# Kernel optimization log

Hardware: AMD Instinct MI355X
Metric: run time of the kernel (lower is better)

## Reference

```python
import jax, jax.numpy as jnp
import numpy as np

B, S, D, H = 4, 2048, 512, 8
DEPTH = D // H


def setup_inputs() -> dict:
    key = jax.random.key(0)
    ks = jax.random.split(key, 12)
    s = 0.02
    return {
        "q": jax.random.normal(ks[0], (B, S, D), jnp.float32),
        "k": jax.random.normal(ks[1], (B, S, D), jnp.float32),
        "v": jax.random.normal(ks[2], (B, S, D), jnp.float32),
        "mask": jax.random.randint(ks[3], (B, 1, 1, S), 0, 2, jnp.int32),
        "wq": jax.random.normal(ks[4], (D, D), jnp.float32) * s,
        "bq": jnp.zeros((D,), jnp.float32),
        "wk": jax.random.normal(ks[5], (D, D), jnp.float32) * s,
        "bk": jnp.zeros((D,), jnp.float32),
        "wv": jax.random.normal(ks[6], (D, D), jnp.float32) * s,
        "bv": jnp.zeros((D,), jnp.float32),
        "wo": jax.random.normal(ks[7], (D, D), jnp.float32) * s,
        "bo": jnp.zeros((D,), jnp.float32),
    }


def _split_heads(x):
    # [B,S,D] -> [B,H,S,depth]
    b = x.shape[0]
    return x.reshape(b, -1, H, DEPTH).transpose(0, 2, 1, 3)


def reference(q, k, v, mask, wq, bq, wk, bk, wv, bv, wo, bo):
    qh = _split_heads(q @ wq + bq)
    kh = _split_heads(k @ wk + bk)
    vh = _split_heads(v @ wv + bv)
    scale = 1.0 / jnp.sqrt(jnp.float32(DEPTH))
    logits = jnp.einsum("bhqd,bhkd->bhqk", qh, kh) * scale
    logits = logits + mask.astype(jnp.float32) * -1e9
    attn = jax.nn.softmax(logits, axis=-1)  # [B,H,Sq,Sk]
    out = jnp.einsum("bhqk,bhkd->bhqd", attn, vh)
    out = out.transpose(0, 2, 1, 3).reshape(q.shape[0], -1, D)
    out = out @ wo + bo
    return out, attn
```

## Files before the change

kernel.cpp:

```cpp
#include <hip/hip_runtime.h>

#define B_ 4
#define S_ 2048
#define D_ 512
#define H_ 8
#define DP_ 64
#define NT_ (S_/64)

typedef __attribute__((ext_vector_type(4))) float f32x4;
typedef __attribute__((ext_vector_type(8))) short short8;
typedef __attribute__((ext_vector_type(4))) int i32x4;

__device__ __forceinline__ short f2bf(float f){
  unsigned u = __float_as_uint(f);
  u += 0x7fff + ((u >> 16) & 1);
  return (short)(u >> 16);
}

__device__ __forceinline__ int cvtpk(float lo, float hi){
  int r;
  asm("v_cvt_pk_bf16_f32 %0, %1, %2" : "=v"(r) : "v"(lo), "v"(hi));
  return r;
}

#define SWZ(r, kb) ((r)*64 + ((kb) ^ (((r)&7)<<3)))
#define F2(r) ((((r)&3)) | ((((r)>>3)&1)<<2))
#define SWZ2(r, kb) ((r)*64 + ((kb) ^ (F2(r)<<3)))

#define WAITV(N) do{ asm volatile("s_waitcnt vmcnt(" #N ")" ::: "memory"); }while(0)
#define BAR() do{ __builtin_amdgcn_s_barrier(); __builtin_amdgcn_sched_barrier(0); }while(0)

template<int NC>
__device__ __forceinline__ void stage_swz(const short* __restrict__ g, int rowStride,
                                          short* shbase, int w, int l){
  #pragma unroll
  for(int i = 0; i < NC; ++i){
    int byte = (w*NC + i)*1024 + l*16;
    int row = byte >> 7;
    int gs = ((byte >> 4) & 7) ^ (row & 7);
    const short* src = g + (size_t)row*rowStride + gs*8;
    __builtin_amdgcn_global_load_lds((const __attribute__((address_space(1))) void*)src,
        (__attribute__((address_space(3))) void*)(shbase + (w*NC + i)*512), 16, 0, 0);
  }
}
template<int NC>
__device__ __forceinline__ void stage_swz2(const short* __restrict__ g, int rowStride,
                                           short* shbase, int w, int l){
  #pragma unroll
  for(int i = 0; i < NC; ++i){
    int byte = (w*NC + i)*1024 + l*16;
    int row = byte >> 7;
    int gs = ((byte >> 4) & 7) ^ F2(row);
    const short* src = g + (size_t)row*rowStride + gs*8;
    __builtin_amdgcn_global_load_lds((const __attribute__((address_space(1))) void*)src,
        (__attribute__((address_space(3))) void*)(shbase + (w*NC + i)*512), 16, 0, 0);
  }
}

__global__ __launch_bounds__(256) void k_pre(const int* __restrict__ mask,
        const float* __restrict__ w0, const float* __restrict__ w1,
        const float* __restrict__ w2, const float* __restrict__ w3,
        short* __restrict__ wT, float* __restrict__ mb){
  __shared__ float tt[32][33];
  const int bi = blockIdx.x, t = threadIdx.x;
  if(bi < 1024){
    const int z = bi >> 8;
    const float* w = z == 0 ? w0 : z == 1 ? w1 : z == 2 ? w2 : w3;
    short* wt = wT + z * 262144;
    const int bxy = bi & 255;
    const int bx = (bxy & 15) * 32, by = (bxy >> 4) * 32;
    const int tx = t & 31, ty = t >> 5;
    #pragma unroll
    for(int i = 0; i < 32; i += 8) tt[ty + i][tx] = w[(by + ty + i) * D_ + bx + tx];
    __syncthreads();
    #pragma unroll
    for(int i = 0; i < 32; i += 8) wt[(bx + ty + i) * D_ + by + tx] = f2bf(tt[tx][ty + i]);
  } else {
    int i = (bi - 1024) * 256 + t;
    mb[i] = mask[i] ? -1.0e9f : 0.0f;
  }
}

__global__ __launch_bounds__(256) void k_gemm_qkv(const float* __restrict__ qf,
        const float* __restrict__ kf, const float* __restrict__ vf,
        const short* __restrict__ WTall, const float* __restrict__ b0,
        const float* __restrict__ b1, const float* __restrict__ b2,
        short* __restrict__ qh, short* __restrict__ kh, short* __restrict__ vvt){
  __shared__ __align__(16) short As[8192];
  __shared__ __align__(16) short Bs[8192];
  const int z = blockIdx.z;
  const float* X = z == 0 ? qf : (z == 1 ? kf : vf);
  const short* WT = WTall + (size_t)z * (D_*D_);
  const float* bias = z==0 ? b0 : (z==1 ? b1 : b2);
  const int t = threadIdx.x, l = t & 63, w = t >> 6;
  const int lr = l & 15, lg = l >> 4;
  const int m0 = blockIdx.x * 128, n0 = blockIdx.y * 128;
  const int wr = w >> 1, wc = w & 1;
  const float* Xb = X + (size_t)m0 * D_;
  const short* Wb = WT + (size_t)n0 * D_;
  f32x4 acc[4][4] = {};
  for(int kt = 0; kt < D_ / 64; ++kt){
    #pragma unroll
    for(int i = 0; i < 4; ++i){
      int e = t + 256 * i;
      int row = e >> 3, c8 = (e & 7) * 8;
      const float* src = Xb + (size_t)row * D_ + kt * 64 + c8;
      float4 f0 = *reinterpret_cast<const float4*>(src);
      float4 f1 = *reinterpret_cast<const float4*>(src + 4);
      i32x4 pk;
      pk[0] = cvtpk(f0.x, f0.y); pk[1] = cvtpk(f0.z, f0.w);
      pk[2] = cvtpk(f1.x, f1.y); pk[3] = cvtpk(f1.z, f1.w);
      *reinterpret_cast<i32x4*>(&As[SWZ(row, c8)]) = pk;
    }
    stage_swz<4>(Wb + kt*64, D_, Bs, w, l);
    __syncthreads();
    #pragma unroll
    for(int ks = 0; ks < 2; ++ks){
      const int kb = ks*32 + lg*8;
      short8 a[4], b[4];
      #pragma unroll
      for(int mt = 0; mt < 4; ++mt)
        a[mt] = *reinterpret_cast<const short8*>(&As[SWZ(wr*64 + mt*16 + lr, kb)]);
      #pragma unroll
      for(int nt = 0; nt < 4; ++nt)
        b[nt] = *reinterpret_cast<const short8*>(&Bs[SWZ(wc*64 + nt*16 + lr, kb)]);
      __builtin_amdgcn_s_setprio(1);
      #pragma unroll
      for(int mt = 0; mt < 4; ++mt)
        #pragma unroll
        for(int nt = 0; nt < 4; ++nt)
          acc[mt][nt] = __builtin_amdgcn_mfma_f32_16x16x32_bf16(a[mt], b[nt], acc[mt][nt], 0, 0, 0);
      __builtin_amdgcn_s_setprio(0);
    }
    __syncthreads();
  }
  #pragma unroll
  for(int mt = 0; mt < 4; ++mt){
    #pragma unroll
    for(int nt = 0; nt < 4; ++nt){
      const int n = n0 + wc*64 + nt*16 + lr;
      const int m4 = m0 + wr*64 + mt*16 + lg*4;
      float vals[4];
      #pragma unroll
      for(int r = 0; r < 4; ++r) vals[r] = acc[mt][nt][r] + bias[n];
      if(z == 2){
        short4 pv4;
        pv4.x = f2bf(vals[0]); pv4.y = f2bf(vals[1]); pv4.z = f2bf(vals[2]); pv4.w = f2bf(vals[3]);
        *reinterpret_cast<short4*>(&vvt[
            (((size_t)((m4 >> 11) * H_ + (n >> 6))) * DP_ + (n & 63)) * S_ + (m4 & 2047)]) = pv4;
      } else {
        short* dst = z == 0 ? qh : kh;
        #pragma unroll
        for(int r = 0; r < 4; ++r){
          int m = m4 + r;
          dst[(((size_t)((m >> 11) * H_ + (n >> 6))) * S_ + (m & 2047)) * DP_ + (n & 63)] = f2bf(vals[r]);
        }
      }
    }
  }
}

__global__ __launch_bounds__(256) void k_gemm_out(const short* __restrict__ X,
        const short* __restrict__ WT, const float* __restrict__ bias,
        float* __restrict__ Out){
  __shared__ __align__(16) short As[8192];
  __shared__ __align__(16) short Bs[8192];
  const int t = threadIdx.x, l = t & 63, w = t >> 6;
  const int lr = l & 15, lg = l >> 4;
  const int m0 = blockIdx.x * 128, n0 = blockIdx.y * 128;
  const int wr = w >> 1, wc = w & 1;
  const short* Xb = X + (size_t)m0 * D_;
  const short* Wb = WT + (size_t)n0 * D_;
  f32x4 acc[4][4] = {};
  for(int kt = 0; kt < D_ / 64; ++kt){
    stage_swz<4>(Xb + kt*64, D_, As, w, l);
    stage_swz<4>(Wb + kt*64, D_, Bs, w, l);
    __syncthreads();
    #pragma unroll
    for(int ks = 0; ks < 2; ++ks){
      const int kb = ks*32 + lg*8;
      short8 a[4], b[4];
      #pragma unroll
      for(int mt = 0; mt < 4; ++mt)
        a[mt] = *reinterpret_cast<const short8*>(&As[SWZ(wr*64 + mt*16 + lr, kb)]);
      #pragma unroll
      for(int nt = 0; nt < 4; ++nt)
        b[nt] = *reinterpret_cast<const short8*>(&Bs[SWZ(wc*64 + nt*16 + lr, kb)]);
      __builtin_amdgcn_s_setprio(1);
      #pragma unroll
      for(int mt = 0; mt < 4; ++mt)
        #pragma unroll
        for(int nt = 0; nt < 4; ++nt)
          acc[mt][nt] = __builtin_amdgcn_mfma_f32_16x16x32_bf16(a[mt], b[nt], acc[mt][nt], 0, 0, 0);
      __builtin_amdgcn_s_setprio(0);
    }
    __syncthreads();
  }
  #pragma unroll
  for(int mt = 0; mt < 4; ++mt){
    #pragma unroll
    for(int nt = 0; nt < 4; ++nt){
      const int n = n0 + wc*64 + nt*16 + lr;
      const int m4 = m0 + wr*64 + mt*16 + lg*4;
      #pragma unroll
      for(int r = 0; r < 4; ++r)
        Out[(size_t)(m4 + r) * D_ + n] = acc[mt][nt][r] + bias[n];
    }
  }
}

__global__ __launch_bounds__(512, 2) void k_attn(const short* __restrict__ qh,
                                                 const short* __restrict__ kh,
                                                 const short* __restrict__ vt,
                                                 const float* __restrict__ mb,
                                                 float* __restrict__ attn,
                                                 short* __restrict__ ctx){
  __shared__ __align__(16) short Sh[45056];
  const int t = threadIdx.x, l = t & 63, w = t >> 6;
  const int lr = l & 15, lg = l >> 4;
  int lin = blockIdx.y * 8 + blockIdx.x;
  int sw = (lin & 7) * 32 + (lin >> 3);
  const int bh = sw >> 3, b = bh >> 3, h = bh & 7;
  const int q0 = (sw & 7) * 256;
  const short* Qb = qh + (size_t)bh * S_ * DP_ + (size_t)q0 * DP_;
  const short* Kb = kh + (size_t)bh * S_ * DP_;
  const short* Vtb = vt + (size_t)bh * DP_ * S_;
  const float* Mbb = mb + b * S_;
  float* Mlds = (float*)Sh;
  short* KA = Sh + 4096;
  short* KB = Sh + 4096;
  short* VB = Sh + 20480;
  short* Qs = Sh + 28672;
  const float scale = 0.125f;

  __builtin_amdgcn_global_load_lds(
      (const __attribute__((address_space(1))) void*)(Mbb + w*256 + l*4),
      (__attribute__((address_space(3))) void*)(Mlds + w*256 + l*4), 16, 0, 0);
  stage_swz2<4>(Qb, DP_, Qs, w, l);
  stage_swz2<1>(Kb,          DP_, KA,          w, l);
  stage_swz2<1>(Kb + 4096,   DP_, KA + 4096,   w, l);
  stage_swz2<1>(Kb + 2*4096, DP_, KA + 2*4096, w, l);
  stage_swz2<1>(Kb + 3*4096, DP_, KA + 3*4096, w, l);
  WAITV(4); BAR();
  short8 bq[2][2];
  #pragma unroll
  for(int qs = 0; qs < 2; ++qs){
    int r = w * 32 + qs * 16 + lr;
    bq[qs][0] = *reinterpret_cast<const short8*>(&Qs[SWZ2(r, lg * 8)]);
    bq[qs][1] = *reinterpret_cast<const short8*>(&Qs[SWZ2(r, 32 + lg * 8)]);
  }
  const int grow = ((lr >> 2) << 3) + (lr & 3);

  float ps[2] = {0.f, 0.f};
  for(int i = 0; i < NT_/2; ++i){
    if(i < NT_/2 - 1){ WAITV(2); } else { WAITV(0); }
    BAR();
    if(i + 2 < NT_/2){
      int tfa = 2*i + 4, tfb = 2*i + 5;
      stage_swz2<1>(Kb + (size_t)tfa * 4096, DP_, KA + (tfa % 6) * 4096, w, l);
      stage_swz2<1>(Kb + (size_t)tfb * 4096, DP_, KA + (tfb % 6) * 4096, w, l);
    }
    #pragma unroll
    for(int tt = 0; tt < 2; ++tt){
      const int kt = 2*i + tt;
      const short* Kc = KA + (kt % 6) * 4096;
      const float* Ml = Mlds + kt * 64;
      #pragma unroll
      for(int st = 0; st < 4; ++st){
        const int ks = st >> 1, h4 = st & 1;
        const int row = grow + h4 * 4 + ks * 32;
        const int mcol = ks * 32 + h4 * 4 + lg * 8;
        const float4 mv = *(const float4*)&Ml[mcol];
        short8 ak0 = *reinterpret_cast<const short8*>(&Kc[SWZ2(row, lg * 8)]);
        short8 ak1 = *reinterpret_cast<const short8*>(&Kc[SWZ2(row, 32 + lg * 8)]);
        __builtin_amdgcn_s_setprio(1);
        f32x4 c0 = {}, c1 = {};
        c0 = __builtin_amdgcn_mfma_f32_16x16x32_bf16(ak0, bq[0][0], c0, 0, 0, 0);
        c0 = __builtin_amdgcn_mfma_f32_16x16x32_bf16(ak1, bq[0][1], c0, 0, 0, 0);
        c1 = __builtin_amdgcn_mfma_f32_16x16x32_bf16(ak0, bq[1][0], c1, 0, 0, 0);
        c1 = __builtin_amdgcn_mfma_f32_16x16x32_bf16(ak1, bq[1][1], c1, 0, 0, 0);
        __builtin_amdgcn_s_setprio(0);
        ps[0] += __expf(__builtin_fmaf(c0[0], scale, mv.x));
        ps[0] += __expf(__builtin_fmaf(c0[1], scale, mv.y));
        ps[0] += __expf(__builtin_fmaf(c0[2], scale, mv.z));
        ps[0] += __expf(__builtin_fmaf(c0[3], scale, mv.w));
        ps[1] += __expf(__builtin_fmaf(c1[0], scale, mv.x));
        ps[1] += __expf(__builtin_fmaf(c1[1], scale, mv.y));
        ps[1] += __expf(__builtin_fmaf(c1[2], scale, mv.z));
        ps[1] += __expf(__builtin_fmaf(c1[3], scale, mv.w));
      }
    }
  }
  #pragma unroll
  for(int qs = 0; qs < 2; ++qs){
    ps[qs] += __shfl_xor(ps[qs], 16, 64);
    ps[qs] += __shfl_xor(ps[qs], 32, 64);
  }
  const float rinv0 = 1.f / ps[0], rinv1 = 1.f / ps[1];

  BAR();
  stage_swz2<1>(Kb,          DP_, KB,          w, l);
  stage_swz2<1>(Kb + 4096,   DP_, KB + 4096,   w, l);
  stage_swz2<1>(Vtb,         S_,  VB,          w, l);
  stage_swz2<1>(Vtb + 64,    S_,  VB + 4096,   w, l);
  stage_swz2<1>(Kb + 2*4096, DP_, KB + 2*4096, w, l);
  stage_swz2<1>(Kb + 3*4096, DP_, KB + 3*4096, w, l);
  stage_swz2<1>(Vtb + 2*64,  S_,  VB + 2*4096, w, l);
  stage_swz2<1>(Vtb + 3*64,  S_,  VB + 3*4096, w, l);

  f32x4 o[2][4] = {};
  for(int i = 0; i < NT_/2; ++i){
    if(i == 0){ WAITV(4); } else { WAITV(16); }
    BAR();
    if(i >= 1 && i + 1 < NT_/2){
      int tfa = 2*i + 2, tfb = 2*i + 3;
      stage_swz2<1>(Kb + (size_t)tfa * 4096, DP_, KB + (tfa & 3) * 4096, w, l);
      stage_swz2<1>(Kb + (size_t)tfb * 4096, DP_, KB + (tfb & 3) * 4096, w, l);
      stage_swz2<1>(Vtb + (size_t)tfa * 64,  S_,  VB + (tfa & 3) * 4096, w, l);
      stage_swz2<1>(Vtb + (size_t)tfb * 64,  S_,  VB + (tfb & 3) * 4096, w, l);
    }
    #pragma unroll
    for(int tt = 0; tt < 2; ++tt){
      const int kt = 2*i + tt;
      const short* Kc = KB + (kt & 3) * 4096;
      const short* Vc = VB + (kt & 3) * 4096;
      const float* Ml = Mlds + kt * 64;
      i32x4 pav[2][2];
      #pragma unroll
      for(int st = 0; st < 4; ++st){
        const int ks = st >> 1, h4 = st & 1;
        const int row = grow + h4 * 4 + ks * 32;
        const int mcol = ks * 32 + h4 * 4 + lg * 8;
        const float4 mv = *(const float4*)&Ml[mcol];
        short8 ak0 = *reinterpret_cast<const short8*>(&Kc[SWZ2(row, lg * 8)]);
        short8 ak1 = *reinterpret_cast<const short8*>(&Kc[SWZ2(row, 32 + lg * 8)]);
        __builtin_amdgcn_s_setprio(1);
        f32x4 c0 = {}, c1 = {};
        c0 = __builtin_amdgcn_mfma_f32_16x16x32_bf16(ak0, bq[0][0], c0, 0, 0, 0);
        c0 = __builtin_amdgcn_mfma_f32_16x16x32_bf16(ak1, bq[0][1], c0, 0, 0, 0);
        c1 = __builtin_amdgcn_mfma_f32_16x16x32_bf16(ak0, bq[1][0], c1, 0, 0, 0);
        c1 = __builtin_amdgcn_mfma_f32_16x16x32_bf16(ak1, bq[1][1], c1, 0, 0, 0);
        __builtin_amdgcn_s_setprio(0);
        float4 pw0, pw1;
        pw0.x = __expf(__builtin_fmaf(c0[0], scale, mv.x)) * rinv0;
        pw0.y = __expf(__builtin_fmaf(c0[1], scale, mv.y)) * rinv0;
        pw0.z = __expf(__builtin_fmaf(c0[2], scale, mv.z)) * rinv0;
        pw0.w = __expf(__builtin_fmaf(c0[3], scale, mv.w)) * rinv0;
        pw1.x = __expf(__builtin_fmaf(c1[0], scale, mv.x)) * rinv1;
        pw1.y = __expf(__builtin_fmaf(c1[1], scale, mv.y)) * rinv1;
        pw1.z = __expf(__builtin_fmaf(c1[2], scale, mv.z)) * rinv1;
        pw1.w = __expf(__builtin_fmaf(c1[3], scale, mv.w)) * rinv1;
        const int q0r = q0 + w * 32 + lr;
        *reinterpret_cast<float4*>(&attn[((size_t)bh * S_ + q0r) * S_ + kt * 64 + mcol]) = pw0;
        *reinterpret_cast<float4*>(&attn[((size_t)bh * S_ + q0r + 16) * S_ + kt * 64 + mcol]) = pw1;
        pav[0][ks][h4 * 2 + 0] = cvtpk(pw0.x, pw0.y);
        pav[0][ks][h4 * 2 + 1] = cvtpk(pw0.z, pw0.w);
        pav[1][ks][h4 * 2 + 0] = cvtpk(pw1.x, pw1.y);
        pav[1][ks][h4 * 2 + 1] = cvtpk(pw1.z, pw1.w);
      }
      #pragma unroll
      for(int ks = 0; ks < 2; ++ks){
        short8 pa0 = __builtin_bit_cast(short8, pav[0][ks]);
        short8 pa1 = __builtin_bit_cast(short8, pav[1][ks]);
        __builtin_amdgcn_s_setprio(1);
        #pragma unroll
        for(int dt = 0; dt < 4; ++dt){
          short8 vb = *reinterpret_cast<const short8*>(&Vc[SWZ2(dt * 16 + lr, ks * 32 + lg * 8)]);
          o[0][dt] = __builtin_amdgcn_mfma_f32_16x16x32_bf16(pa0, vb, o[0][dt], 0, 0, 0);
          o[1][dt] = __builtin_amdgcn_mfma_f32_16x16x32_bf16(pa1, vb, o[1][dt], 0, 0, 0);
        }
        __builtin_amdgcn_s_setprio(0);
      }
    }
  }
  #pragma unroll
  for(int qs = 0; qs < 2; ++qs){
    #pragma unroll
    for(int dt = 0; dt < 4; ++dt){
      #pragma unroll
      for(int r = 0; r < 4; ++r){
        int q = q0 + w * 32 + qs * 16 + lg * 4 + r;
        int dd = h * 64 + dt * 16 + lr;
        ctx[((size_t)b * S_ + q) * D_ + dd] = f2bf(o[qs][dt][r]);
      }
    }
  }
}

extern "C" void kernel_launch(void* const* d_in, const int* in_sizes, int n_in,
                              void* d_out, int out_size, void* d_ws, size_t ws_size,
                              hipStream_t stream){
  const float* q  = (const float*)d_in[0];
  const float* k  = (const float*)d_in[1];
  const float* v  = (const float*)d_in[2];
  const int* mask = (const int*)d_in[3];
  const float* wq = (const float*)d_in[4];
  const float* bq = (const float*)d_in[5];
  const float* wk = (const float*)d_in[6];
  const float* bk = (const float*)d_in[7];
  const float* wv = (const float*)d_in[8];
  const float* bv = (const float*)d_in[9];
  const float* wo = (const float*)d_in[10];
  const float* bo = (const float*)d_in[11];

  float* out  = (float*)d_out;
  float* attn = out + (size_t)B_ * S_ * D_;

  char* ws = (char*)d_ws;
  short* qh  = (short*)(ws);
  short* kh  = (short*)(ws + 8388608);
  short* vvt = (short*)(ws + 16777216);
  short* ctx = (short*)(ws + 25165824);
  short* wT  = (short*)(ws + 33554432);
  float* mb  = (float*)(ws + 33554432 + 4 * 524288);

  hipLaunchKernelGGL(k_pre, dim3(1056), dim3(256), 0, stream,
                     mask, wq, wk, wv, wo, wT, mb);

  hipLaunchKernelGGL(k_gemm_qkv, dim3(64, 4, 3), dim3(256), 0, stream,
                     q, k, v, wT, bq, bk, bv, qh, kh, vvt);

  hipLaunchKernelGGL(k_attn, dim3(8, 32), dim3(512), 0, stream, qh, kh, vvt, mb, attn, ctx);

  hipLaunchKernelGGL(k_gemm_out, dim3(64, 4), dim3(256), 0, stream, ctx, wT + 3 * 262144, bo, out);
}
```

Before: 251.5 us.

## Split key tiles across two warp groups and halve query tile per block

The attention kernel now processes 128 queries per block instead of 256. Its 8 warps form two groups that take alternating key tiles, so twice as many blocks launch. Row-sum partials and the output accumulators are combined across the two groups through LDS. The launch bound rises to 4 blocks per CU and LDS use drops. The aim is better occupancy and more parallelism across CUs, at the cost of extra LDS reductions, barriers and redundant K/V staging per block.

Result: faster. 223.0 us (-11.3%).

```diff
diff --git a/kernel.cpp b/kernel.cpp
--- a/kernel.cpp
+++ b/kernel.cpp
@@ -28,6 +28,7 @@
 #define SWZ2(r, kb) ((r)*64 + ((kb) ^ (F2(r)<<3)))
 
 #define WAITV(N) do{ asm volatile("s_waitcnt vmcnt(" #N ")" ::: "memory"); }while(0)
+#define WAITLGKM() do{ asm volatile("s_waitcnt lgkmcnt(0)" ::: "memory"); }while(0)
 #define BAR() do{ __builtin_amdgcn_s_barrier(); __builtin_amdgcn_sched_barrier(0); }while(0)
 
 template<int NC>
@@ -209,19 +210,20 @@
   }
 }
 
-__global__ __launch_bounds__(512, 2) void k_attn(const short* __restrict__ qh,
+__global__ __launch_bounds__(512, 4) void k_attn(const short* __restrict__ qh,
                                                  const short* __restrict__ kh,
                                                  const short* __restrict__ vt,
                                                  const float* __restrict__ mb,
                                                  float* __restrict__ attn,
                                                  short* __restrict__ ctx){
-  __shared__ __align__(16) short Sh[45056];
+  __shared__ __align__(16) short Sh[37376];
   const int t = threadIdx.x, l = t & 63, w = t >> 6;
   const int lr = l & 15, lg = l >> 4;
-  int lin = blockIdx.y * 8 + blockIdx.x;
-  int sw = (lin & 7) * 32 + (lin >> 3);
-  const int bh = sw >> 3, b = bh >> 3, h = bh & 7;
-  const int q0 = (sw & 7) * 256;
+  const int wq = w & 3, g = w >> 2;
+  int lin = blockIdx.y * 16 + blockIdx.x;
+  int sw = (lin & 7) * 64 + (lin >> 3);
+  const int bh = sw >> 4, b = bh >> 3, h = bh & 7;
+  const int q0 = (sw & 15) * 128;
   const short* Qb = qh + (size_t)bh * S_ * DP_ + (size_t)q0 * DP_;
   const short* Kb = kh + (size_t)bh * S_ * DP_;
   const short* Vtb = vt + (size_t)bh * DP_ * S_;
@@ -231,12 +233,13 @@
   short* KB = Sh + 4096;
   short* VB = Sh + 20480;
   short* Qs = Sh + 28672;
+  float* Ps_ = (float*)(Sh + 36864);
   const float scale = 0.125f;
 
   __builtin_amdgcn_global_load_lds(
       (const __attribute__((address_space(1))) void*)(Mbb + w*256 + l*4),
       (__attribute__((address_space(3))) void*)(Mlds + w*256 + l*4), 16, 0, 0);
-  stage_swz2<4>(Qb, DP_, Qs, w, l);
+  stage_swz2<2>(Qb, DP_, Qs, w, l);
   stage_swz2<1>(Kb,          DP_, KA,          w, l);
   stage_swz2<1>(Kb + 4096,   DP_, KA + 4096,   w, l);
   stage_swz2<1>(Kb + 2*4096, DP_, KA + 2*4096, w, l);
@@ -245,13 +248,13 @@
   short8 bq[2][2];
   #pragma unroll
   for(int qs = 0; qs < 2; ++qs){
-    int r = w * 32 + qs * 16 + lr;
+    int r = wq * 32 + qs * 16 + lr;
     bq[qs][0] = *reinterpret_cast<const short8*>(&Qs[SWZ2(r, lg * 8)]);
     bq[qs][1] = *reinterpret_cast<const short8*>(&Qs[SWZ2(r, 32 + lg * 8)]);
   }
   const int grow = ((lr >> 2) << 3) + (lr & 3);
 
-  float ps[2] = {0.f, 0.f};
+  float ps2[2] = {0.f, 0.f};
   for(int i = 0; i < NT_/2; ++i){
     if(i < NT_/2 - 1){ WAITV(2); } else { WAITV(0); }
     BAR();
@@ -260,45 +263,42 @@
       stage_swz2<1>(Kb + (size_t)tfa * 4096, DP_, KA + (tfa % 6) * 4096, w, l);
       stage_swz2<1>(Kb + (size_t)tfb * 4096, DP_, KA + (tfb % 6) * 4096, w, l);
     }
-    #pragma unroll
-    for(int tt = 0; tt < 2; ++tt){
-      const int kt = 2*i + tt;
-      const short* Kc = KA + (kt % 6) * 4096;
-      const float* Ml = Mlds + kt * 64;
-      #pragma unroll
-      for(int st = 0; st < 4; ++st){
-        const int ks = st >> 1, h4 = st & 1;
-        const int row = grow + h4 * 4 + ks * 32;
-        const int mcol = ks * 32 + h4 * 4 + lg * 8;
-        const float4 mv = *(const float4*)&Ml[mcol];
-        short8 ak0 = *reinterpret_cast<const short8*>(&Kc[SWZ2(row, lg * 8)]);
-        short8 ak1 = *reinterpret_cast<const short8*>(&Kc[SWZ2(row, 32 + lg * 8)]);
-        __builtin_amdgcn_s_setprio(1);
-        f32x4 c0 = {}, c1 = {};
-        c0 = __builtin_amdgcn_mfma_f32_16x16x32_bf16(ak0, bq[0][0], c0, 0, 0, 0);
-        c0 = __builtin_amdgcn_mfma_f32_16x16x32_bf16(ak1, bq[0][1], c0, 0, 0, 0);
-        c1 = __builtin_amdgcn_mfma_f32_16x16x32_bf16(ak0, bq[1][0], c1, 0, 0, 0);
-        c1 = __builtin_amdgcn_mfma_f32_16x16x32_bf16(ak1, bq[1][1], c1, 0, 0, 0);
-        __builtin_amdgcn_s_setprio(0);
-        ps[0] += __expf(__builtin_fmaf(c0[0], scale, mv.x));
-        ps[0] += __expf(__builtin_fmaf(c0[1], scale, mv.y));
-        ps[0] += __expf(__builtin_fmaf(c0[2], scale, mv.z));
-        ps[0] += __expf(__builtin_fmaf(c0[3], scale, mv.w));
-        ps[1] += __expf(__builtin_fmaf(c1[0], scale, mv.x));
-        ps[1] += __expf(__builtin_fmaf(c1[1], scale, mv.y));
-        ps[1] += __expf(__builtin_fmaf(c1[2], scale, mv.z));
-        ps[1] += __expf(__builtin_fmaf(c1[3], scale, mv.w));
-      }
+    const int kt = 2*i + g;
+    const short* Kc = KA + (kt % 6) * 4096;
+    const float* Ml = Mlds + kt * 64;
+    #pragma unroll
+    for(int st = 0; st < 4; ++st){
+      const int ks = st >> 1, h4 = st & 1;
+      const int row = grow + h4 * 4 + ks * 32;
+      const int mcol = ks * 32 + h4 * 4 + lg * 8;
+      const float4 mv = *(const float4*)&Ml[mcol];
+      short8 ak0 = *reinterpret_cast<const short8*>(&Kc[SWZ2(row, lg * 8)]);
+      short8 ak1 = *reinterpret_cast<const short8*>(&Kc[SWZ2(row, 32 + lg * 8)]);
+      __builtin_amdgcn_s_setprio(1);
+      f32x4 c0 = {}, c1 = {};
+      c0 = __builtin_amdgcn_mfma_f32_16x16x32_bf16(ak0, bq[0][0], c0, 0, 0, 0);
+      c0 = __builtin_amdgcn_mfma_f32_16x16x32_bf16(ak1, bq[0][1], c0, 0, 0, 0);
+      c1 = __builtin_amdgcn_mfma_f32_16x16x32_bf16(ak0, bq[1][0], c1, 0, 0, 0);
+      c1 = __builtin_amdgcn_mfma_f32_16x16x32_bf16(ak1, bq[1][1], c1, 0, 0, 0);
+      __builtin_amdgcn_s_setprio(0);
+      ps2[0] += __expf(__builtin_fmaf(c0[0], scale, mv.x));
+      ps2[0] += __expf(__builtin_fmaf(c0[1], scale, mv.y));
+      ps2[0] += __expf(__builtin_fmaf(c0[2], scale, mv.z));
+      ps2[0] += __expf(__builtin_fmaf(c0[3], scale, mv.w));
+      ps2[1] += __expf(__builtin_fmaf(c1[0], scale, mv.x));
+      ps2[1] += __expf(__builtin_fmaf(c1[1], scale, mv.y));
+      ps2[1] += __expf(__builtin_fmaf(c1[2], scale, mv.z));
+      ps2[1] += __expf(__builtin_fmaf(c1[3], scale, mv.w));
     }
   }
   #pragma unroll
   for(int qs = 0; qs < 2; ++qs){
-    ps[qs] += __shfl_xor(ps[qs], 16, 64);
-    ps[qs] += __shfl_xor(ps[qs], 32, 64);
-  }
-  const float rinv0 = 1.f / ps[0], rinv1 = 1.f / ps[1];
-
-  BAR();
+    ps2[qs] += __shfl_xor(ps2[qs], 16, 64);
+    ps2[qs] += __shfl_xor(ps2[qs], 32, 64);
+  }
+  Ps_[(w*2 + 0)*16 + lr] = ps2[0];
+  Ps_[(w*2 + 1)*16 + lr] = ps2[1];
+  WAITLGKM(); BAR();
   stage_swz2<1>(Kb,          DP_, KB,          w, l);
   stage_swz2<1>(Kb + 4096,   DP_, KB + 4096,   w, l);
   stage_swz2<1>(Vtb,         S_,  VB,          w, l);
@@ -307,10 +307,12 @@
   stage_swz2<1>(Kb + 3*4096, DP_, KB + 3*4096, w, l);
   stage_swz2<1>(Vtb + 2*64,  S_,  VB + 2*4096, w, l);
   stage_swz2<1>(Vtb + 3*64,  S_,  VB + 3*4096, w, l);
+  const float rinv0 = 1.f / (ps2[0] + Ps_[((w^4)*2 + 0)*16 + lr]);
+  const float rinv1 = 1.f / (ps2[1] + Ps_[((w^4)*2 + 1)*16 + lr]);
 
   f32x4 o[2][4] = {};
   for(int i = 0; i < NT_/2; ++i){
-    if(i == 0){ WAITV(4); } else { WAITV(16); }
+    if(i == 0){ WAITV(4); } else { WAITV(8); }
     BAR();
     if(i >= 1 && i + 1 < NT_/2){
       int tfa = 2*i + 2, tfb = 2*i + 3;
@@ -319,69 +321,82 @@
       stage_swz2<1>(Vtb + (size_t)tfa * 64,  S_,  VB + (tfa & 3) * 4096, w, l);
       stage_swz2<1>(Vtb + (size_t)tfb * 64,  S_,  VB + (tfb & 3) * 4096, w, l);
     }
-    #pragma unroll
-    for(int tt = 0; tt < 2; ++tt){
-      const int kt = 2*i + tt;
-      const short* Kc = KB + (kt & 3) * 4096;
-      const short* Vc = VB + (kt & 3) * 4096;
-      const float* Ml = Mlds + kt * 64;
-      i32x4 pav[2][2];
-      #pragma unroll
-      for(int st = 0; st < 4; ++st){
-        const int ks = st >> 1, h4 = st & 1;
-        const int row = grow + h4 * 4 + ks * 32;
-        const int mcol = ks * 32 + h4 * 4 + lg * 8;
-        const float4 mv = *(const float4*)&Ml[mcol];
-        short8 ak0 = *reinterpret_cast<const short8*>(&Kc[SWZ2(row, lg * 8)]);
-        short8 ak1 = *reinterpret_cast<const short8*>(&Kc[SWZ2(row, 32 + lg * 8)]);
-        __builtin_amdgcn_s_setprio(1);
-        f32x4 c0 = {}, c1 = {};
-        c0 = __builtin_amdgcn_mfma_f32_16x16x32_bf16(ak0, bq[0][0], c0, 0, 0, 0);
-        c0 = __builtin_amdgcn_mfma_f32_16x16x32_bf16(ak1, bq[0][1], c0, 0, 0, 0);
-        c1 = __builtin_amdgcn_mfma_f32_16x16x32_bf16(ak0, bq[1][0], c1, 0, 0, 0);
-        c1 = __builtin_amdgcn_mfma_f32_16x16x32_bf16(ak1, bq[1][1], c1, 0, 0, 0);
-        __builtin_amdgcn_s_setprio(0);
-        float4 pw0, pw1;
-        pw0.x = __expf(__builtin_fmaf(c0[0], scale, mv.x)) * rinv0;
-        pw0.y = __expf(__builtin_fmaf(c0[1], scale, mv.y)) * rinv0;
-        pw0.z = __expf(__builtin_fmaf(c0[2], scale, mv.z)) * rinv0;
-        pw0.w = __expf(__builtin_fmaf(c0[3], scale, mv.w)) * rinv0;
-        pw1.x = __expf(__builtin_fmaf(c1[0], scale, mv.x)) * rinv1;
-        pw1.y = __expf(__builtin_fmaf(c1[1], scale, mv.y)) * rinv1;
-        pw1.z = __expf(__builtin_fmaf(c1[2], scale, mv.z)) * rinv1;
-        pw1.w = __expf(__builtin_fmaf(c1[3], scale, mv.w)) * rinv1;
-        const int q0r = q0 + w * 32 + lr;
-        *reinterpret_cast<float4*>(&attn[((size_t)bh * S_ + q0r) * S_ + kt * 64 + mcol]) = pw0;
-        *reinterpret_cast<float4*>(&attn[((size_t)bh * S_ + q0r + 16) * S_ + kt * 64 + mcol]) = pw1;
-        pav[0][ks][h4 * 2 + 0] = cvtpk(pw0.x, pw0.y);
-        pav[0][ks][h4 * 2 + 1] = cvtpk(pw0.z, pw0.w);
-        pav[1][ks][h4 * 2 + 0] = cvtpk(pw1.x, pw1.y);
-        pav[1][ks][h4 * 2 + 1] = cvtpk(pw1.z, pw1.w);
+    const int kt = 2*i + g;
+    const short* Kc = KB + (kt & 3) * 4096;
+    const short* Vc = VB + (kt & 3) * 4096;
+    const float* Ml = Mlds + kt * 64;
+    i32x4 pav[2][2];
+    #pragma unroll
+    for(int st = 0; st < 4; ++st){
+      const int ks = st >> 1, h4 = st & 1;
+      const int row = grow + h4 * 4 + ks * 32;
+      const int mcol = ks * 32 + h4 * 4 + lg * 8;
+      const float4 mv = *(const float4*)&Ml[mcol];
+      short8 ak0 = *reinterpret_cast<const short8*>(&Kc[SWZ2(row, lg * 8)]);
+      short8 ak1 = *reinterpret_cast<const short8*>(&Kc[SWZ2(row, 32 + lg * 8)]);
+      __builtin_amdgcn_s_setprio(1);
+      f32x4 c0 = {}, c1 = {};
+      c0 = __builtin_amdgcn_mfma_f32_16x16x32_bf16(ak0, bq[0][0], c0, 0, 0, 0);
+      c0 = __builtin_amdgcn_mfma_f32_16x16x32_bf16(ak1, bq[0][1], c0, 0, 0, 0);
+      c1 = __builtin_amdgcn_mfma_f32_16x16x32_bf16(ak0, bq[1][0], c1, 0, 0, 0);
+      c1 = __builtin_amdgcn_mfma_f32_16x16x32_bf16(ak1, bq[1][1], c1, 0, 0, 0);
+      __builtin_amdgcn_s_setprio(0);
+      float4 pw0, pw1;
+      pw0.x = __expf(__builtin_fmaf(c0[0], scale, mv.x)) * rinv0;
+      pw0.y = __expf(__builtin_fmaf(c0[1], scale, mv.y)) * rinv0;
+      pw0.z = __expf(__builtin_fmaf(c0[2], scale, mv.z)) * rinv0;
+      pw0.w = __expf(__builtin_fmaf(c0[3], scale, mv.w)) * rinv0;
+      pw1.x = __expf(__builtin_fmaf(c1[0], scale, mv.x)) * rinv1;
+      pw1.y = __expf(__builtin_fmaf(c1[1], scale, mv.y)) * rinv1;
+      pw1.z = __expf(__builtin_fmaf(c1[2], scale, mv.z)) * rinv1;
+      pw1.w = __expf(__builtin_fmaf(c1[3], scale, mv.w)) * rinv1;
+      const int qr = q0 + wq * 32 + lr;
+      *reinterpret_cast<float4*>(&attn[((size_t)bh * S_ + qr) * S_ + kt * 64 + mcol]) = pw0;
+      *reinterpret_cast<float4*>(&attn[((size_t)bh * S_ + qr + 16) * S_ + kt * 64 + mcol]) = pw1;
+      pav[0][ks][h4 * 2 + 0] = cvtpk(pw0.x, pw0.y);
+      pav[0][ks][h4 * 2 + 1] = cvtpk(pw0.z, pw0.w);
+      pav[1][ks][h4 * 2 + 0] = cvtpk(pw1.x, pw1.y);
+      pav[1][ks][h4 * 2 + 1] = cvtpk(pw1.z, pw1.w);
+    }
+    #pragma unroll
+    for(int ks = 0; ks < 2; ++ks){
+      short8 pa0 = __builtin_bit_cast(short8, pav[0][ks]);
+      short8 pa1 = __builtin_bit_cast(short8, pav[1][ks]);
+      __builtin_amdgcn_s_setprio(1);
+      #pragma unroll
+      for(int dt = 0; dt < 4; ++dt){
+        short8 vb = *reinterpret_cast<const short8*>(&Vc[SWZ2(dt * 16 + lr, ks * 32 + lg * 8)]);
+        o[0][dt] = __builtin_amdgcn_mfma_f32_16x16x32_bf16(pa0, vb, o[0][dt], 0, 0, 0);
+        o[1][dt] = __builtin_amdgcn_mfma_f32_16x16x32_bf16(pa1, vb, o[1][dt], 0, 0, 0);
       }
-      #pragma unroll
-      for(int ks = 0; ks < 2; ++ks){
-        short8 pa0 = __builtin_bit_cast(short8, pav[0][ks]);
-        short8 pa1 = __builtin_bit_cast(short8, pav[1][ks]);
-        __builtin_amdgcn_s_setprio(1);
+      __builtin_amdgcn_s_setprio(0);
+    }
+  }
+
+  BAR();
+  float* Oc = (float*)(Sh + 4096);
+  if(g == 0){
+    #pragma unroll
+    for(int qs = 0; qs < 2; ++qs)
+      #pragma unroll
+      for(int dt = 0; dt < 4; ++dt)
         #pragma unroll
-        for(int dt = 0; dt < 4; ++dt){
-          short8 vb = *reinterpret_cast<const short8*>(&Vc[SWZ2(dt * 16 + lr, ks * 32 + lg * 8)]);
-          o[0][dt] = __builtin_amdgcn_mfma_f32_16x16x32_bf16(pa0, vb, o[0][dt], 0, 0, 0);
-          o[1][dt] = __builtin_amdgcn_mfma_f32_16x16x32_bf16(pa1, vb, o[1][dt], 0, 0, 0);
+        for(int r = 0; r < 4; ++r)
+          Oc[(wq*32 + qs*16 + lg*4 + r) * 65 + dt*16 + lr] = o[qs][dt][r];
+  }
+  WAITLGKM(); BAR();
+  if(g == 1){
+    #pragma unroll
+    for(int qs = 0; qs < 2; ++qs){
+      #pragma unroll
+      for(int dt = 0; dt < 4; ++dt){
+        #pragma unroll
+        for(int r = 0; r < 4; ++r){
+          float v = o[qs][dt][r] + Oc[(wq*32 + qs*16 + lg*4 + r) * 65 + dt*16 + lr];
+          int qg = q0 + wq*32 + qs*16 + lg*4 + r;
+          int dd = h * 64 + dt * 16 + lr;
+          ctx[((size_t)b * S_ + qg) * D_ + dd] = f2bf(v);
         }
-        __builtin_amdgcn_s_setprio(0);
-      }
-    }
-  }
-  #pragma unroll
-  for(int qs = 0; qs < 2; ++qs){
-    #pragma unroll
-    for(int dt = 0; dt < 4; ++dt){
-      #pragma unroll
-      for(int r = 0; r < 4; ++r){
-        int q = q0 + w * 32 + qs * 16 + lg * 4 + r;
-        int dd = h * 64 + dt * 16 + lr;
-        ctx[((size_t)b * S_ + q) * D_ + dd] = f2bf(o[qs][dt][r]);
       }
     }
   }
@@ -420,7 +435,7 @@
   hipLaunchKernelGGL(k_gemm_qkv, dim3(64, 4, 3), dim3(256), 0, stream,
                      q, k, v, wT, bq, bk, bv, qh, kh, vvt);
 
-  hipLaunchKernelGGL(k_attn, dim3(8, 32), dim3(512), 0, stream, qh, kh, vvt, mb, attn, ctx);
+  hipLaunchKernelGGL(k_attn, dim3(16, 32), dim3(512), 0, stream, qh, kh, vvt, mb, attn, ctx);
 
   hipLaunchKernelGGL(k_gemm_out, dim3(64, 4), dim3(256), 0, stream, ctx, wT + 3 * 262144, bo, out);
 }
```
